# Performance work log

Hardware: AMD Instinct MI355X
Metric: run time of the kernel (lower is better)

Reference implementation:

```python
import jax, jax.numpy as jnp
import numpy as np

B, SQ, SC, D = 16, 1024, 1024, 768
H = 2 * D  # 1536, fc width
NCLS = 2


def setup_inputs() -> dict:
    key = jax.random.key(0)
    ks = jax.random.split(key, 8)
    q = jax.random.normal(ks[0], (B, SQ, D), jnp.float32)
    c = jax.random.normal(ks[1], (B, SC, D), jnp.float32)
    mask_q = jax.random.randint(ks[2], (B, SQ), 0, 2).astype(jnp.int32)
    mask_c = jax.random.randint(ks[3], (B, SC), 0, 2).astype(jnp.int32)
    labels = jax.random.randint(ks[4], (B,), 0, NCLS)
    # torch nn.Linear convention: weight [out, in], y = x @ W.T + b
    W1 = jax.random.normal(ks[5], (H, H), jnp.float32) * 0.02
    b1 = jnp.zeros((H,), jnp.float32)
    W2 = jax.random.normal(ks[6], (NCLS, H), jnp.float32) * 0.02
    b2 = jnp.zeros((NCLS,), jnp.float32)
    return dict(q=q, c=c, mask_q=mask_q, mask_c=mask_c, labels=labels,
                W1=W1, b1=b1, W2=W2, b2=b2)


def reference(q, c, mask_q, mask_c, labels, W1, b1, W2, b2):
    # masked QK^T score matrix: [B, SQ, SC]
    s = jnp.einsum('bik,bjk->bij', q, c)
    s = s * mask_q[:, :, None].astype(s.dtype) * mask_c[:, None, :].astype(s.dtype)
    s = jnp.where(s == 0.0, -jnp.inf, s)  # x[x == 0.0] = -inf
    p = jnp.nan_to_num(jax.nn.softmax(s, axis=2))   # softmax over context axis
    pp = jnp.nan_to_num(jax.nn.softmax(s, axis=1))  # softmax over question axis
    a = jnp.einsum('bjk,bij->bk', c, p)   # weighted combine into context feats
    bb = jnp.einsum('bik,bij->bk', q, pp)  # weighted combine into question feats
    x = jnp.concatenate([a, bb], axis=1)  # [B, 1536]
    x = jnp.tanh(x @ W1.T + b1)           # fc1 + tanh (dropout = identity in eval)
    logits = x @ W2.T + b2                # fc2
    logp = jax.nn.log_softmax(logits, axis=1)  # LogSoftmax(dim=1)
    # NLLLoss (mean reduction)
    loss = -jnp.mean(jnp.take_along_axis(logp, labels[:, None], axis=1))
    return (loss, logp)
```

## Files before the change

kernel.cpp:

```cpp
#include <hip/hip_runtime.h>
#include <math.h>

#define B_   16
#define SQ_  1024
#define SC_  1024
#define D_   768
#define H_   1536
#define BK   64
#define LDK  72

typedef __attribute__((ext_vector_type(4))) float f32x4;
typedef __attribute__((ext_vector_type(8))) short bf16x8;

__device__ __forceinline__ unsigned cvtpk(float x, float y) {
  unsigned r;
  asm("v_cvt_pk_bf16_f32 %0, %1, %2" : "=v"(r) : "v"(x), "v"(y));
  return r;
}

__global__ __launch_bounds__(256) void compact_kernel(
    const int* __restrict__ mask_q, const int* __restrict__ mask_c,
    int* __restrict__ idx_q, int* __restrict__ idx_c, int* __restrict__ cnt)
{
  int which = blockIdx.x & 1;
  int b     = blockIdx.x >> 1;
  const int* m = (which ? mask_c : mask_q) + b * 1024;
  int* idx     = (which ? idx_c : idx_q) + b * 1024;

  __shared__ int tsum[256];
  int t = threadIdx.x;
  int v[4], s = 0;
#pragma unroll
  for (int e = 0; e < 4; ++e) { v[e] = (m[t * 4 + e] != 0) ? 1 : 0; s += v[e]; }
  tsum[t] = s;
  __syncthreads();
  for (int off = 1; off < 256; off <<= 1) {
    int add = (t >= off) ? tsum[t - off] : 0;
    __syncthreads();
    tsum[t] += add;
    __syncthreads();
  }
  int pos = tsum[t] - s;
#pragma unroll
  for (int e = 0; e < 4; ++e) {
    if (v[e]) idx[pos++] = t * 4 + e;
  }
  if (t == 255) cnt[b * 2 + which] = tsum[255];
}

__global__ __launch_bounds__(256) void gemm_mfma_kernel(
    const float* __restrict__ q, const float* __restrict__ c,
    const int* __restrict__ idx_q, const int* __restrict__ idx_c,
    const int* __restrict__ cnt, float* __restrict__ S)
{
  __shared__ unsigned short Ah[64][LDK];
  __shared__ unsigned short Al[64][LDK];
  __shared__ unsigned short Bh[64][LDK];
  __shared__ unsigned short Bl[64][LDK];

  const int b  = blockIdx.z;
  const int i0 = blockIdx.y * 64;
  const int j0 = blockIdx.x * 64;
  const int nq = cnt[2 * b], nc = cnt[2 * b + 1];
  if (i0 >= nq || j0 >= nc) return;

  const int t    = threadIdx.x;
  const int lane = t & 63;
  const int w    = t >> 6;

  const int srow = t >> 2;
  const int kq4  = (t & 3) * 4;
  const int fr   = lane & 15;
  const int fq   = lane >> 4;
  const int kg   = fq * 8;

  const int rq = idx_q[b * 1024 + min(i0 + srow, nq - 1)];
  const int rc = idx_c[b * 1024 + min(j0 + srow, nc - 1)];
  const float* qrowP = q + ((size_t)b * SQ_ + rq) * D_;
  const float* crowP = c + ((size_t)b * SC_ + rc) * D_;

  f32x4 acc[4] = {};

  for (int k0 = 0; k0 < D_; k0 += BK) {
    uint2 aH[4], aL[4], bH[4], bL[4];
#pragma unroll
    for (int ch = 0; ch < 4; ++ch) {
      int koff = k0 + kq4 + ch * 16;
      float4 av = *(const float4*)(qrowP + koff);
      float4 bv = *(const float4*)(crowP + koff);
      unsigned h01 = cvtpk(av.x, av.y);
      unsigned h23 = cvtpk(av.z, av.w);
      float h0 = __uint_as_float(h01 << 16);
      float h1 = __uint_as_float(h01 & 0xFFFF0000u);
      float h2 = __uint_as_float(h23 << 16);
      float h3 = __uint_as_float(h23 & 0xFFFF0000u);
      aH[ch] = make_uint2(h01, h23);
      aL[ch] = make_uint2(cvtpk(av.x - h0, av.y - h1), cvtpk(av.z - h2, av.w - h3));
      unsigned g01 = cvtpk(bv.x, bv.y);
      unsigned g23 = cvtpk(bv.z, bv.w);
      float g0 = __uint_as_float(g01 << 16);
      float g1 = __uint_as_float(g01 & 0xFFFF0000u);
      float g2 = __uint_as_float(g23 << 16);
      float g3 = __uint_as_float(g23 & 0xFFFF0000u);
      bH[ch] = make_uint2(g01, g23);
      bL[ch] = make_uint2(cvtpk(bv.x - g0, bv.y - g1), cvtpk(bv.z - g2, bv.w - g3));
    }
    __syncthreads();
#pragma unroll
    for (int ch = 0; ch < 4; ++ch) {
      int koff = kq4 + ch * 16;
      *(uint2*)&Ah[srow][koff] = aH[ch];
      *(uint2*)&Al[srow][koff] = aL[ch];
      *(uint2*)&Bh[srow][koff] = bH[ch];
      *(uint2*)&Bl[srow][koff] = bL[ch];
    }
    __syncthreads();

#pragma unroll
    for (int ksub = 0; ksub < 2; ++ksub) {
      const int kg2 = kg + ksub * 32;
      bf16x8 b_h = *reinterpret_cast<const bf16x8*>(&Bh[w * 16 + fr][kg2]);
      bf16x8 b_l = *reinterpret_cast<const bf16x8*>(&Bl[w * 16 + fr][kg2]);
#pragma unroll
      for (int m = 0; m < 4; ++m) {
        bf16x8 a_h = *reinterpret_cast<const bf16x8*>(&Ah[m * 16 + fr][kg2]);
        bf16x8 a_l = *reinterpret_cast<const bf16x8*>(&Al[m * 16 + fr][kg2]);
        acc[m] = __builtin_amdgcn_mfma_f32_16x16x32_bf16(a_h, b_h, acc[m], 0, 0, 0);
        acc[m] = __builtin_amdgcn_mfma_f32_16x16x32_bf16(a_h, b_l, acc[m], 0, 0, 0);
        acc[m] = __builtin_amdgcn_mfma_f32_16x16x32_bf16(a_l, b_h, acc[m], 0, 0, 0);
      }
    }
  }

  const int col = j0 + w * 16 + fr;
  const bool cok = (col < nc);
#pragma unroll
  for (int m = 0; m < 4; ++m) {
    int rbase = i0 + m * 16 + fq * 4;
    float* Sp = S + ((size_t)b * SQ_ + rbase) * SC_ + col;
#pragma unroll
    for (int rr = 0; rr < 4; ++rr) {
      float v = acc[m][rr];
      bool valid = ((rbase + rr) < nq) && cok && (v != 0.f);
      Sp[(size_t)rr * SC_] = valid ? v : -INFINITY;
    }
  }
}

__global__ __launch_bounds__(256) void row_stats_kernel(
    const float* __restrict__ S, const int* __restrict__ cnt,
    float* __restrict__ rmE, float* __restrict__ riE)
{
  int w    = threadIdx.x >> 6;
  int lane = threadIdx.x & 63;
  int row  = blockIdx.x * 4 + w;
  int b = row >> 10, i = row & 1023;
  int nq_pad = (cnt[2 * b] + 63) & ~63;
  if (i >= nq_pad) return;
  int nc_pad = (cnt[2 * b + 1] + 63) & ~63;
  const float4* Sr = (const float4*)(S + (size_t)row * SC_);

  float m = -INFINITY, s = 0.f;
  int n4 = nc_pad >> 2;
  for (int j4 = lane; j4 < n4; j4 += 64) {
    float4 v = Sr[j4];
    float vm = fmaxf(fmaxf(v.x, v.y), fmaxf(v.z, v.w));
    if (vm > m) { s *= __expf(m - vm); m = vm; }
    if (m > -INFINITY) {
      s += __expf(v.x - m) + __expf(v.y - m) + __expf(v.z - m) + __expf(v.w - m);
    }
  }
#pragma unroll
  for (int o = 32; o; o >>= 1) {
    float om = __shfl_xor(m, o);
    float os = __shfl_xor(s, o);
    float nm = fmaxf(m, om);
    float e1 = (m == nm) ? 1.f : __expf(m - nm);
    float e2 = (om == nm) ? 1.f : __expf(om - nm);
    s = s * e1 + os * e2;
    m = nm;
  }
  if (lane == 0) {
    bool dead = !(s > 0.f);
    rmE[row] = dead ? INFINITY : m;
    riE[row] = dead ? 0.f : 1.0f / s;
  }
}

__global__ __launch_bounds__(1024) void col_pass_kernel(
    const float* __restrict__ S, const int* __restrict__ cnt,
    const float* __restrict__ rmE, const float* __restrict__ riE,
    float* __restrict__ cmE, float* __restrict__ ciE,
    float* __restrict__ colsum_p)
{
  __shared__ float redm[1024], reds[1024], redp[1024];

  int b  = blockIdx.y;
  int j0 = blockIdx.x * 64;
  int nq_pad = (cnt[2 * b] + 63) & ~63;
  int nc_pad = (cnt[2 * b + 1] + 63) & ~63;
  if (j0 >= nc_pad) return;
  int t  = threadIdx.x;

  int j     = j0 + (t & 63);
  int wv    = t >> 6;
  int chunk = nq_pad >> 4;
  int i0    = wv * chunk;
  const float* Sb  = S + ((size_t)b * SQ_ + i0) * SC_ + j;
  const float* rmb = rmE + b * SQ_ + i0;
  const float* rib = riE + b * SQ_ + i0;

  float cm = -INFINITY, cs = 0.f, cp = 0.f;
  for (int ii = 0; ii < chunk; ++ii) {
    float v = Sb[(size_t)ii * SC_];
    cp += __expf(v - rmb[ii]) * rib[ii];
    if (v > cm) { cs = cs * __expf(cm - v) + 1.0f; cm = v; }
    else if (cm > -INFINITY) cs += __expf(v - cm);
  }

  redm[t] = cm; reds[t] = cs; redp[t] = cp;
  __syncthreads();
  if (t < 64) {
    float m = redm[t], s = reds[t], p = redp[t];
#pragma unroll
    for (int wv2 = 1; wv2 < 16; ++wv2) {
      float om = redm[wv2 * 64 + t], os = reds[wv2 * 64 + t];
      float nm = fmaxf(m, om);
      float e1 = (m == nm) ? 1.f : __expf(m - nm);
      float e2 = (om == nm) ? 1.f : __expf(om - nm);
      s = s * e1 + os * e2; m = nm;
      p += redp[wv2 * 64 + t];
    }
    bool dead = !(s > 0.f);
    cmE[b * SC_ + j0 + t] = dead ? INFINITY : m;
    ciE[b * SC_ + j0 + t] = dead ? 0.f : 1.0f / s;
    colsum_p[b * SC_ + j0 + t] = p;
  }
}

__global__ __launch_bounds__(256) void rowsum_pp_kernel(
    const float* __restrict__ S, const int* __restrict__ cnt,
    const float* __restrict__ cmE, const float* __restrict__ ciE,
    float* __restrict__ rowsum_pp)
{
  int t = threadIdx.x;
  int row0 = blockIdx.x * 4;
  int b = row0 >> 10;
  int nq = cnt[2 * b];
  if ((row0 & 1023) >= nq) return;
  int nc_pad = (cnt[2 * b + 1] + 63) & ~63;

  int w = t >> 6, lane = t & 63;
  int row = row0 + w;
  const float4* Sr  = (const float4*)(S + (size_t)row * SC_);
  const float4* cm4 = (const float4*)(cmE + b * SC_);
  const float4* ci4 = (const float4*)(ciE + b * SC_);

  float accv = 0.f;
  int n4 = nc_pad >> 2;
  for (int j4 = lane; j4 < n4; j4 += 64) {
    float4 v = Sr[j4];
    float4 cm = cm4[j4];
    float4 ci = ci4[j4];
    accv += __expf(v.x - cm.x) * ci.x;
    accv += __expf(v.y - cm.y) * ci.y;
    accv += __expf(v.z - cm.z) * ci.z;
    accv += __expf(v.w - cm.w) * ci.w;
  }
#pragma unroll
  for (int o = 32; o; o >>= 1) accv += __shfl_xor(accv, o);
  if (lane == 0) rowsum_pp[row] = accv;
}

__global__ __launch_bounds__(256) void combine_kernel(
    const float* __restrict__ q, const float* __restrict__ c,
    const int* __restrict__ idx_q, const int* __restrict__ idx_c,
    const int* __restrict__ cnt,
    const float* __restrict__ colsum_p, const float* __restrict__ rowsum_pp,
    float* __restrict__ Xp)
{
  int jc = blockIdx.x;
  int op = blockIdx.y;
  int b  = blockIdx.z;
  int t  = threadIdx.x;

  int n = op ? cnt[2 * b] : cnt[2 * b + 1];
  const float* src = op ? (q + (size_t)b * SQ_ * D_) : (c + (size_t)b * SC_ * D_);
  const float* wv  = op ? (rowsum_pp + b * SQ_) : (colsum_p + b * SC_);
  const int*   idx = (op ? idx_q : idx_c) + b * 1024;

  float a0 = 0.f, a1 = 0.f, a2 = 0.f;
  int je = min(jc * 32 + 32, n);
  for (int j = jc * 32; j < je; ++j) {
    float wj = wv[j];
    const float* r = src + (size_t)idx[j] * D_;
    a0 += wj * r[t];
    a1 += wj * r[t + 256];
    a2 += wj * r[t + 512];
  }
  float* xp = Xp + ((size_t)jc * B_ + b) * H_ + op * D_;
  xp[t] = a0; xp[t + 256] = a1; xp[t + 512] = a2;
}

__global__ __launch_bounds__(256) void reduce_x_kernel(
    const float* __restrict__ Xp, float* __restrict__ X)
{
  int idx = blockIdx.x * 256 + threadIdx.x;
  float s = 0.f;
#pragma unroll
  for (int ch = 0; ch < 32; ++ch) s += Xp[(size_t)ch * B_ * H_ + idx];
  X[idx] = s;
}

__global__ __launch_bounds__(256) void fc1_kernel(
    const float* __restrict__ X, const float* __restrict__ W1,
    const float* __restrict__ b1, float* __restrict__ Y)
{
  int w = threadIdx.x >> 6, lane = threadIdx.x & 63;
  int gw = blockIdx.x * 4 + w;
  int b = gw & 15;
  int h = gw >> 4;
  const float4* x  = (const float4*)(X + (size_t)b * H_);
  const float4* wr = (const float4*)(W1 + (size_t)h * H_);
  float accv = 0.f;
#pragma unroll
  for (int it = 0; it < 6; ++it) {
    int idx = it * 64 + lane;
    float4 xv = x[idx], wv = wr[idx];
    accv += xv.x * wv.x + xv.y * wv.y + xv.z * wv.z + xv.w * wv.w;
  }
#pragma unroll
  for (int o = 32; o; o >>= 1) accv += __shfl_xor(accv, o);
  if (lane == 0) Y[(size_t)b * H_ + h] = tanhf(accv + b1[h]);
}

__global__ __launch_bounds__(64) void fc2_loss_kernel(
    const float* __restrict__ Y, const float* __restrict__ W2,
    const float* __restrict__ b2, const int* __restrict__ labels,
    float* __restrict__ out)
{
  __shared__ float logp_s[B_][2];
  int t = threadIdx.x;
  if (t < 2 * B_) {
    int b = t >> 1, n = t & 1;
    const float* y = Y + (size_t)b * H_;
    const float* w = W2 + (size_t)n * H_;
    float accv = b2[n];
    for (int k = 0; k < H_; ++k) accv += y[k] * w[k];
    logp_s[b][n] = accv;
  }
  __syncthreads();
  if (t < B_) {
    float l0 = logp_s[t][0], l1 = logp_s[t][1];
    float m = fmaxf(l0, l1);
    float lse = m + logf(expf(l0 - m) + expf(l1 - m));
    logp_s[t][0] = l0 - lse;
    logp_s[t][1] = l1 - lse;
  }
  __syncthreads();
  if (t < 2 * B_) out[1 + t] = logp_s[t >> 1][t & 1];
  if (t == 0) {
    float loss = 0.f;
    for (int b = 0; b < B_; ++b) loss -= logp_s[b][labels[b]];
    out[0] = loss / (float)B_;
  }
}

extern "C" void kernel_launch(void* const* d_in, const int* in_sizes, int n_in,
                              void* d_out, int out_size, void* d_ws, size_t ws_size,
                              hipStream_t stream) {
  const float* q      = (const float*)d_in[0];
  const float* c      = (const float*)d_in[1];
  const int*   mask_q = (const int*)d_in[2];
  const int*   mask_c = (const int*)d_in[3];
  const int*   labels = (const int*)d_in[4];
  const float* W1     = (const float*)d_in[5];
  const float* b1     = (const float*)d_in[6];
  const float* W2     = (const float*)d_in[7];
  const float* b2     = (const float*)d_in[8];
  float* out = (float*)d_out;

  float* ws        = (float*)d_ws;
  float* S         = ws;
  float* rmE       = ws + (size_t)B_ * SQ_ * SC_;
  float* riE       = rmE + B_ * SQ_;
  float* cmE       = riE + B_ * SQ_;
  float* ciE       = cmE + B_ * SC_;
  float* colsum_p  = ciE + B_ * SC_;
  float* rowsum_pp = colsum_p + B_ * SC_;
  int*   cnt       = (int*)(rowsum_pp + B_ * SQ_);
  int*   idx_q     = cnt + 2 * B_;
  int*   idx_c     = idx_q + B_ * SQ_;
  float* Xp        = ws;
  float* X         = ws + 32 * B_ * H_;
  float* Y         = X + B_ * H_;

  compact_kernel<<<2 * B_, 256, 0, stream>>>(mask_q, mask_c, idx_q, idx_c, cnt);

  dim3 g1(SC_ / 64, SQ_ / 64, B_);
  gemm_mfma_kernel<<<g1, 256, 0, stream>>>(q, c, idx_q, idx_c, cnt, S);

  row_stats_kernel<<<(B_ * SQ_) / 4, 256, 0, stream>>>(S, cnt, rmE, riE);
  col_pass_kernel<<<dim3(SC_ / 64, B_), 1024, 0, stream>>>(S, cnt, rmE, riE,
                                                           cmE, ciE, colsum_p);
  rowsum_pp_kernel<<<(B_ * SQ_) / 4, 256, 0, stream>>>(S, cnt, cmE, ciE, rowsum_pp);

  combine_kernel<<<dim3(32, 2, B_), 256, 0, stream>>>(q, c, idx_q, idx_c, cnt,
                                                      colsum_p, rowsum_pp, Xp);
  reduce_x_kernel<<<(B_ * H_) / 256, 256, 0, stream>>>(Xp, X);
  fc1_kernel<<<(B_ * H_) / 4, 256, 0, stream>>>(X, W1, b1, Y);
  fc2_loss_kernel<<<1, 64, 0, stream>>>(Y, W2, b2, labels, out);
}
```

Measured before the change: 180.9 us.

## Double-buffer split-bf16 GEMM tiles and reuse W1 rows across batch in fc1

The score GEMM now uses a two-stage shared-memory ping-pong with BK halved to 32. Global loads for the next K tile are issued before the MFMAs on the current tile, and the split-and-store happens after them, so each K step needs one barrier instead of two. Separately, fc1 keeps one W1 row in registers per wave and loops over all 16 batch rows, so W1 is read once rather than once per batch element. The trade-offs are more loop iterations with less work per barrier in the GEMM, and fewer fc1 blocks with a serial loop over the batch.

```diff
diff --git a/kernel.cpp b/kernel.cpp
--- a/kernel.cpp
+++ b/kernel.cpp
@@ -6,8 +6,8 @@
 #define SC_  1024
 #define D_   768
 #define H_   1536
-#define BK   64
-#define LDK  72
+#define BK   32
+#define LDK  40
 
 typedef __attribute__((ext_vector_type(4))) float f32x4;
 typedef __attribute__((ext_vector_type(8))) short bf16x8;
@@ -16,6 +16,17 @@
   unsigned r;
   asm("v_cvt_pk_bf16_f32 %0, %1, %2" : "=v"(r) : "v"(x), "v"(y));
   return r;
+}
+
+__device__ __forceinline__ void split4(float4 v, uint2& hi, uint2& lo) {
+  unsigned h01 = cvtpk(v.x, v.y);
+  unsigned h23 = cvtpk(v.z, v.w);
+  float h0 = __uint_as_float(h01 << 16);
+  float h1 = __uint_as_float(h01 & 0xFFFF0000u);
+  float h2 = __uint_as_float(h23 << 16);
+  float h3 = __uint_as_float(h23 & 0xFFFF0000u);
+  hi = make_uint2(h01, h23);
+  lo = make_uint2(cvtpk(v.x - h0, v.y - h1), cvtpk(v.z - h2, v.w - h3));
 }
 
 __global__ __launch_bounds__(256) void compact_kernel(
@@ -53,10 +64,10 @@
     const int* __restrict__ idx_q, const int* __restrict__ idx_c,
     const int* __restrict__ cnt, float* __restrict__ S)
 {
-  __shared__ unsigned short Ah[64][LDK];
-  __shared__ unsigned short Al[64][LDK];
-  __shared__ unsigned short Bh[64][LDK];
-  __shared__ unsigned short Bl[64][LDK];
+  __shared__ unsigned short Ah[2][64][LDK];
+  __shared__ unsigned short Al[2][64][LDK];
+  __shared__ unsigned short Bh[2][64][LDK];
+  __shared__ unsigned short Bl[2][64][LDK];
 
   const int b  = blockIdx.z;
   const int i0 = blockIdx.y * 64;
@@ -69,7 +80,7 @@
   const int w    = t >> 6;
 
   const int srow = t >> 2;
-  const int kq4  = (t & 3) * 4;
+  const int kc   = (t & 3) * 4;
   const int fr   = lane & 15;
   const int fq   = lane >> 4;
   const int kg   = fq * 8;
@@ -81,55 +92,51 @@
 
   f32x4 acc[4] = {};
 
+  float4 av0 = *(const float4*)(qrowP + kc);
+  float4 av1 = *(const float4*)(qrowP + kc + 16);
+  float4 bv0 = *(const float4*)(crowP + kc);
+  float4 bv1 = *(const float4*)(crowP + kc + 16);
+  {
+    uint2 hi, lo;
+    split4(av0, hi, lo); *(uint2*)&Ah[0][srow][kc]      = hi; *(uint2*)&Al[0][srow][kc]      = lo;
+    split4(av1, hi, lo); *(uint2*)&Ah[0][srow][kc + 16] = hi; *(uint2*)&Al[0][srow][kc + 16] = lo;
+    split4(bv0, hi, lo); *(uint2*)&Bh[0][srow][kc]      = hi; *(uint2*)&Bl[0][srow][kc]      = lo;
+    split4(bv1, hi, lo); *(uint2*)&Bh[0][srow][kc + 16] = hi; *(uint2*)&Bl[0][srow][kc + 16] = lo;
+  }
+  __syncthreads();
+
+  int cur = 0;
   for (int k0 = 0; k0 < D_; k0 += BK) {
-    uint2 aH[4], aL[4], bH[4], bL[4];
-#pragma unroll
-    for (int ch = 0; ch < 4; ++ch) {
-      int koff = k0 + kq4 + ch * 16;
-      float4 av = *(const float4*)(qrowP + koff);
-      float4 bv = *(const float4*)(crowP + koff);
-      unsigned h01 = cvtpk(av.x, av.y);
-      unsigned h23 = cvtpk(av.z, av.w);
-      float h0 = __uint_as_float(h01 << 16);
-      float h1 = __uint_as_float(h01 & 0xFFFF0000u);
-      float h2 = __uint_as_float(h23 << 16);
-      float h3 = __uint_as_float(h23 & 0xFFFF0000u);
-      aH[ch] = make_uint2(h01, h23);
-      aL[ch] = make_uint2(cvtpk(av.x - h0, av.y - h1), cvtpk(av.z - h2, av.w - h3));
-      unsigned g01 = cvtpk(bv.x, bv.y);
-      unsigned g23 = cvtpk(bv.z, bv.w);
-      float g0 = __uint_as_float(g01 << 16);
-      float g1 = __uint_as_float(g01 & 0xFFFF0000u);
-      float g2 = __uint_as_float(g23 << 16);
-      float g3 = __uint_as_float(g23 & 0xFFFF0000u);
-      bH[ch] = make_uint2(g01, g23);
-      bL[ch] = make_uint2(cvtpk(bv.x - g0, bv.y - g1), cvtpk(bv.z - g2, bv.w - g3));
+    const int next = k0 + BK;
+    const bool has_next = (next < D_);
+    if (has_next) {
+      av0 = *(const float4*)(qrowP + next + kc);
+      av1 = *(const float4*)(qrowP + next + kc + 16);
+      bv0 = *(const float4*)(crowP + next + kc);
+      bv1 = *(const float4*)(crowP + next + kc + 16);
+    }
+
+    bf16x8 b_h = *reinterpret_cast<const bf16x8*>(&Bh[cur][w * 16 + fr][kg]);
+    bf16x8 b_l = *reinterpret_cast<const bf16x8*>(&Bl[cur][w * 16 + fr][kg]);
+#pragma unroll
+    for (int m = 0; m < 4; ++m) {
+      bf16x8 a_h = *reinterpret_cast<const bf16x8*>(&Ah[cur][m * 16 + fr][kg]);
+      bf16x8 a_l = *reinterpret_cast<const bf16x8*>(&Al[cur][m * 16 + fr][kg]);
+      acc[m] = __builtin_amdgcn_mfma_f32_16x16x32_bf16(a_h, b_h, acc[m], 0, 0, 0);
+      acc[m] = __builtin_amdgcn_mfma_f32_16x16x32_bf16(a_h, b_l, acc[m], 0, 0, 0);
+      acc[m] = __builtin_amdgcn_mfma_f32_16x16x32_bf16(a_l, b_h, acc[m], 0, 0, 0);
+    }
+
+    if (has_next) {
+      int nxt = cur ^ 1;
+      uint2 hi, lo;
+      split4(av0, hi, lo); *(uint2*)&Ah[nxt][srow][kc]      = hi; *(uint2*)&Al[nxt][srow][kc]      = lo;
+      split4(av1, hi, lo); *(uint2*)&Ah[nxt][srow][kc + 16] = hi; *(uint2*)&Al[nxt][srow][kc + 16] = lo;
+      split4(bv0, hi, lo); *(uint2*)&Bh[nxt][srow][kc]      = hi; *(uint2*)&Bl[nxt][srow][kc]      = lo;
+      split4(bv1, hi, lo); *(uint2*)&Bh[nxt][srow][kc + 16] = hi; *(uint2*)&Bl[nxt][srow][kc + 16] = lo;
     }
     __syncthreads();
-#pragma unroll
-    for (int ch = 0; ch < 4; ++ch) {
-      int koff = kq4 + ch * 16;
-      *(uint2*)&Ah[srow][koff] = aH[ch];
-      *(uint2*)&Al[srow][koff] = aL[ch];
-      *(uint2*)&Bh[srow][koff] = bH[ch];
-      *(uint2*)&Bl[srow][koff] = bL[ch];
-    }
-    __syncthreads();
-
-#pragma unroll
-    for (int ksub = 0; ksub < 2; ++ksub) {
-      const int kg2 = kg + ksub * 32;
-      bf16x8 b_h = *reinterpret_cast<const bf16x8*>(&Bh[w * 16 + fr][kg2]);
-      bf16x8 b_l = *reinterpret_cast<const bf16x8*>(&Bl[w * 16 + fr][kg2]);
-#pragma unroll
-      for (int m = 0; m < 4; ++m) {
-        bf16x8 a_h = *reinterpret_cast<const bf16x8*>(&Ah[m * 16 + fr][kg2]);
-        bf16x8 a_l = *reinterpret_cast<const bf16x8*>(&Al[m * 16 + fr][kg2]);
-        acc[m] = __builtin_amdgcn_mfma_f32_16x16x32_bf16(a_h, b_h, acc[m], 0, 0, 0);
-        acc[m] = __builtin_amdgcn_mfma_f32_16x16x32_bf16(a_h, b_l, acc[m], 0, 0, 0);
-        acc[m] = __builtin_amdgcn_mfma_f32_16x16x32_bf16(a_l, b_h, acc[m], 0, 0, 0);
-      }
-    }
+    cur ^= 1;
   }
 
   const int col = j0 + w * 16 + fr;
@@ -317,21 +324,25 @@
     const float* __restrict__ b1, float* __restrict__ Y)
 {
   int w = threadIdx.x >> 6, lane = threadIdx.x & 63;
-  int gw = blockIdx.x * 4 + w;
-  int b = gw & 15;
-  int h = gw >> 4;
-  const float4* x  = (const float4*)(X + (size_t)b * H_);
+  int h = blockIdx.x * 4 + w;
   const float4* wr = (const float4*)(W1 + (size_t)h * H_);
-  float accv = 0.f;
-#pragma unroll
-  for (int it = 0; it < 6; ++it) {
-    int idx = it * 64 + lane;
-    float4 xv = x[idx], wv = wr[idx];
-    accv += xv.x * wv.x + xv.y * wv.y + xv.z * wv.z + xv.w * wv.w;
-  }
-#pragma unroll
-  for (int o = 32; o; o >>= 1) accv += __shfl_xor(accv, o);
-  if (lane == 0) Y[(size_t)b * H_ + h] = tanhf(accv + b1[h]);
+  float4 wv[6];
+#pragma unroll
+  for (int it = 0; it < 6; ++it) wv[it] = wr[it * 64 + lane];
+  float bias = b1[h];
+
+  for (int b = 0; b < B_; ++b) {
+    const float4* x = (const float4*)(X + (size_t)b * H_);
+    float accv = 0.f;
+#pragma unroll
+    for (int it = 0; it < 6; ++it) {
+      float4 xv = x[it * 64 + lane];
+      accv += xv.x * wv[it].x + xv.y * wv[it].y + xv.z * wv[it].z + xv.w * wv[it].w;
+    }
+#pragma unroll
+    for (int o = 32; o; o >>= 1) accv += __shfl_xor(accv, o);
+    if (lane == 0) Y[(size_t)b * H_ + h] = tanhf(accv + bias);
+  }
 }
 
 __global__ __launch_bounds__(64) void fc2_loss_kernel(
@@ -408,6 +419,6 @@
   combine_kernel<<<dim3(32, 2, B_), 256, 0, stream>>>(q, c, idx_q, idx_c, cnt,
                                                       colsum_p, rowsum_pp, Xp);
   reduce_x_kernel<<<(B_ * H_) / 256, 256, 0, stream>>>(Xp, X);
-  fc1_kernel<<<(B_ * H_) / 4, 256, 0, stream>>>(X, W1, b1, Y);
+  fc1_kernel<<<H_ / 4, 256, 0, stream>>>(X, W1, b1, Y);
   fc2_loss_kernel<<<1, 64, 0, stream>>>(Y, W2, b2, labels, out);
 }
```

After: 158.4 us. 12.4% less time.
